# Kernel optimization log

Measured on AMD Instinct MI355X. Metric: run time of the kernel, lower is better.

The kernel has to match this reference:

```python
import jax, jax.numpy as jnp
import numpy as np

B = 64
IN_FEATURES = 20000
OUT_FEATURES = 2000  # out_features * K with K=1
N_EDGES = 2_000_000


def setup_inputs() -> dict:
    key = jax.random.key(0)
    k1, k2, k3 = jax.random.split(key, 3)
    input = jax.random.normal(k1, (B, IN_FEATURES), dtype=jnp.float32)
    # col 0: input neuron index, col 1: output neuron index (both < 2000, valid for both ranges)
    sparse_mask = jax.random.randint(k2, (N_EDGES, 2), 0, OUT_FEATURES, dtype=jnp.int64)
    weight = jax.random.normal(k3, (N_EDGES,), dtype=jnp.float32)
    bias = jnp.zeros((OUT_FEATURES,), dtype=jnp.float32)
    return {"input": input, "sparse_mask": sparse_mask, "weight": weight, "bias": bias}


def reference(input, sparse_mask, weight, bias):
    # gather: [B, E]
    src = input[:, sparse_mask[:, 0]] * weight[None, :]
    # scatter-add per-edge contributions into output neurons
    out = jnp.zeros((input.shape[0], OUT_FEATURES), dtype=input.dtype)
    out = out.at[:, sparse_mask[:, 1]].add(src)
    return out + bias
```

## Files before the change

### kernel.cpp

```cpp
#include <hip/hip_runtime.h>


#define ROWS8 8
#define NB 256
#define NSEGP 512
#define SCAP 32
#define OVB 32
#define E_PT 8
#define TPB_SC 512
#define SEGX (TPB_SC * E_PT)
#define PAD32 0xFFFFFFFFu

#define TILE_O 64
#define KS 64
#define SLICES 16
#define PSTRIDE 2048

__global__ __launch_bounds__(TPB_SC) void smw_scatter13(
    const int* __restrict__ mask, const float* __restrict__ wgt,
    unsigned* __restrict__ binned, int* __restrict__ counts,
    int2* __restrict__ ovfblk, int n_edges, int krows, int nbins, int nseg) {
    __shared__ int hist[NB];
    __shared__ int sflag;
    __shared__ int ovfc;
    extern __shared__ unsigned stage32[];
    const int tid = threadIdx.x;
    const int blk = blockIdx.x;
    const long long e0 = (long long)blk * SEGX;
    if (tid < NB) hist[tid] = 0;
    if (tid == 0) ovfc = 0;
    if (tid < 64) {
        unsigned v = (tid < n_edges) ? ((const unsigned*)mask)[2 * tid + 1] : 0u;
        unsigned long long bal = __ballot(v != 0u);
        if (tid == 0) sflag = (bal == 0ull) ? 1 : 0;
    }
    __syncthreads();
    const bool is64 = (sflag != 0);

    int ci[E_PT], co[E_PT]; float wv[E_PT];
    if (is64) {
        #pragma unroll
        for (int i = 0; i < E_PT; ++i) {
            long long e = e0 + (long long)i * TPB_SC + tid;
            ci[i] = -1; co[i] = 0;
            if (e < n_edges) { int4 mm = ((const int4*)mask)[e]; ci[i] = mm.x; co[i] = mm.z; }
        }
    } else {
        #pragma unroll
        for (int i = 0; i < E_PT; ++i) {
            long long e = e0 + (long long)i * TPB_SC + tid;
            ci[i] = -1; co[i] = 0;
            if (e < n_edges) { int2 mm = ((const int2*)mask)[e]; ci[i] = mm.x; co[i] = mm.y; }
        }
    }
    #pragma unroll
    for (int i = 0; i < E_PT; ++i) {
        long long e = e0 + (long long)i * TPB_SC + tid;
        wv[i] = (e < n_edges) ? wgt[e] : 0.0f;
    }

    #pragma unroll
    for (int i = 0; i < E_PT; ++i) {
        if ((unsigned)ci[i] < (unsigned)krows) {
            int b = ci[i] >> 3;
            int r = atomicAdd(&hist[b], 1);
            if (r < SCAP) {
                unsigned u  = __float_as_uint(wv[i]);
                unsigned bf = (u + 0x7FFFu + ((u >> 16) & 1u)) >> 16;
                unsigned key = (((unsigned)(ci[i] & 7)) << 11) | (unsigned)(co[i] & 0x7FF);
                stage32[b * SCAP + r] = (key << 16) | bf;
            } else {
                int j = atomicAdd(&ovfc, 1);
                if (j < OVB)
                    ovfblk[blk * OVB + j] =
                        make_int2((ci[i] << 16) | (co[i] & 0xFFFF),
                                  __float_as_int(wv[i]));
            }
        }
    }
    __syncthreads();
    const int grp = tid >> 4;
    const int ln  = tid & 15;
    for (int b = grp; b < nbins; b += (TPB_SC / 16)) {
        int c = hist[b]; if (c > SCAP) c = SCAP;
        int cp = (c + 7) & ~7;
        long long base = ((long long)b * nseg + blk) * SCAP;
        for (int k = ln; k < cp; k += 16)
            binned[base + k] = (k < c) ? stage32[b * SCAP + k] : PAD32;
        if (ln == 0) counts[b * NSEGP + blk] = cp;
    }
    if (tid == 0) {
        int oc = ovfc; if (oc > OVB) oc = OVB;
        counts[(NB - 1) * NSEGP + blk] = oc;
    }
}

__global__ __launch_bounds__(512) void smw_bin_build10(
    const unsigned* __restrict__ binned, const int* __restrict__ counts,
    const int2* __restrict__ ovfblk, float* __restrict__ W,
    int out_f, int krows, int nseg) {
    extern __shared__ float tile[];
    const int tid = threadIdx.x;
    const int bin = blockIdx.x;
    const int tile_elems = ROWS8 * out_f;
    {
        float4* t4 = (float4*)tile;
        int n4 = tile_elems >> 2;
        for (int t = tid; t < n4; t += 512) t4[t] = make_float4(0.f, 0.f, 0.f, 0.f);
    }
    __syncthreads();
    const int grp = tid >> 3;
    const int ln8 = tid & 7;
    for (int s = grp; s < nseg; s += 64) {
        int cp = counts[bin * NSEGP + s];
        const uint4* sp = (const uint4*)(binned + ((long long)bin * nseg + s) * SCAP);
        for (int j = ln8; j * 4 < cp; j += 8) {
            uint4 q = sp[j];
            #pragma unroll
            for (int t = 0; t < 4; ++t) {
                unsigned r = (t == 0) ? q.x : (t == 1) ? q.y : (t == 2) ? q.z : q.w;
                if ((int)r >= 0) {
                    unsigned key = r >> 16;
                    atomicAdd(&tile[(int)(key >> 11) * out_f + (int)(key & 0x7FFu)],
                              __uint_as_float((r & 0xFFFFu) << 16));
                }
            }
        }
    }
    for (int s = tid; s < nseg; s += 512) {
        int oc = counts[(NB - 1) * NSEGP + s];
        for (int j = 0; j < oc; ++j) {
            int2 r = ovfblk[s * OVB + j];
            int ci = ((unsigned)r.x) >> 16;
            if ((ci >> 3) == bin)
                atomicAdd(&tile[(ci & 7) * out_f + (r.x & 0xFFFF)],
                          __int_as_float(r.y));
        }
    }
    __syncthreads();
    #pragma unroll
    for (int r = 0; r < ROWS8; ++r) {
        int row = bin * ROWS8 + r;
        if (row >= krows) break;
        float* dst = W + (long long)row * out_f;
        const float* s = tile + r * out_f;
        for (int c = tid * 4; c < out_f; c += 2048)
            *(float4*)&dst[c] = *(const float4*)&s[c];
    }
}

__device__ __forceinline__ void smw_load_a(float4 (&r)[4], const float* __restrict__ A,
                                           int k0, int in_features, int krows,
                                           int Bsz, int tid) {
    #pragma unroll
    for (int t = 0; t < 4; ++t) {
        int idx = t * 256 + tid;
        int b = idx >> 4;
        int c4 = (idx & 15) * 4;
        int gi = k0 + c4;
        float4 v = make_float4(0.f, 0.f, 0.f, 0.f);
        if (b < Bsz) {
            const float* src = A + (long long)b * in_features + gi;
            if (gi + 3 < krows) v = *(const float4*)src;
            else {
                if (gi + 0 < krows) v.x = src[0];
                if (gi + 1 < krows) v.y = src[1];
                if (gi + 2 < krows) v.z = src[2];
                if (gi + 3 < krows) v.w = src[3];
            }
        }
        r[t] = v;
    }
}

__device__ __forceinline__ void smw_load_w(float4 (&r)[4], const float* __restrict__ W,
                                           int k0, int o_base, int out_f, int krows,
                                           int tid) {
    #pragma unroll
    for (int t = 0; t < 4; ++t) {
        int idx = t * 256 + tid;
        int rr = idx >> 4;
        int c4 = (idx & 15) * 4;
        int gi = k0 + rr;
        int go = o_base + c4;
        float4 v = make_float4(0.f, 0.f, 0.f, 0.f);
        if (gi < krows) {
            const float* src = W + (long long)gi * out_f + go;
            if (go + 3 < out_f) v = *(const float4*)src;
            else {
                if (go + 0 < out_f) v.x = src[0];
                if (go + 1 < out_f) v.y = src[1];
                if (go + 2 < out_f) v.z = src[2];
                if (go + 3 < out_f) v.w = src[3];
            }
        }
        r[t] = v;
    }
}

__global__ __launch_bounds__(256) void smw_gemm6(
    const float* __restrict__ A, const float* __restrict__ W,
    float* __restrict__ partial, int in_features, int out_f, int krows, int Bsz) {
    __shared__ float As[64][KS + 4];
    __shared__ float Ws[KS][TILE_O];
    const int tid = threadIdx.x;
    const int tx = tid & 15;
    const int ty = tid >> 4;
    const int o_base = blockIdx.x * TILE_O;
    const int k0a = blockIdx.y * 2 * KS;
    const int k0b = k0a + KS;

    float4 ra[4], rw[4];
    smw_load_a(ra, A, k0a, in_features, krows, Bsz, tid);
    smw_load_w(rw, W, k0a, o_base, out_f, krows, tid);
    #pragma unroll
    for (int t = 0; t < 4; ++t) {
        int idx = t * 256 + tid;
        *(float4*)&As[idx >> 4][(idx & 15) * 4] = ra[t];
        *(float4*)&Ws[idx >> 4][(idx & 15) * 4] = rw[t];
    }
    smw_load_a(ra, A, k0b, in_features, krows, Bsz, tid);
    smw_load_w(rw, W, k0b, o_base, out_f, krows, tid);
    __syncthreads();

    float acc[4][4] = {};
    #pragma unroll 8
    for (int i = 0; i < KS; ++i) {
        float4 w4 = *(const float4*)&Ws[i][tx * 4];
        float a[4];
        #pragma unroll
        for (int r = 0; r < 4; ++r) a[r] = As[ty * 4 + r][i];
        #pragma unroll
        for (int r = 0; r < 4; ++r) {
            acc[r][0] += a[r] * w4.x;
            acc[r][1] += a[r] * w4.y;
            acc[r][2] += a[r] * w4.z;
            acc[r][3] += a[r] * w4.w;
        }
    }
    __syncthreads();
    #pragma unroll
    for (int t = 0; t < 4; ++t) {
        int idx = t * 256 + tid;
        *(float4*)&As[idx >> 4][(idx & 15) * 4] = ra[t];
        *(float4*)&Ws[idx >> 4][(idx & 15) * 4] = rw[t];
    }
    __syncthreads();
    #pragma unroll 8
    for (int i = 0; i < KS; ++i) {
        float4 w4 = *(const float4*)&Ws[i][tx * 4];
        float a[4];
        #pragma unroll
        for (int r = 0; r < 4; ++r) a[r] = As[ty * 4 + r][i];
        #pragma unroll
        for (int r = 0; r < 4; ++r) {
            acc[r][0] += a[r] * w4.x;
            acc[r][1] += a[r] * w4.y;
            acc[r][2] += a[r] * w4.z;
            acc[r][3] += a[r] * w4.w;
        }
    }

    float* P = partial + (long long)blockIdx.y * 64 * PSTRIDE;
    #pragma unroll
    for (int r = 0; r < 4; ++r) {
        int b = ty * 4 + r;
        if (b < Bsz)
            *(float4*)&P[(long long)b * PSTRIDE + o_base + tx * 4] =
                make_float4(acc[r][0], acc[r][1], acc[r][2], acc[r][3]);
    }
}

__global__ void smw_reduce3(const float* __restrict__ partial,
                            const float* __restrict__ bias,
                            float* __restrict__ out, int out_f, int Bsz, int total4) {
    int idx = blockIdx.x * blockDim.x + threadIdx.x;
    if (idx >= total4) return;
    const int of4 = out_f >> 2;
    int b = idx / of4, o4 = idx - b * of4;
    const float4* B4 = (const float4*)bias;
    const float4* P4 = (const float4*)partial;
    float4 acc = B4[o4];
    #pragma unroll
    for (int s = 0; s < SLICES; ++s) {
        float4 v = P4[((long long)s * 64 + b) * (PSTRIDE >> 2) + o4];
        acc.x += v.x; acc.y += v.y; acc.z += v.z; acc.w += v.w;
    }
    ((float4*)out)[idx] = acc;
}

__global__ void smw_detect(const unsigned int* __restrict__ m, int* __restrict__ flag) {
    if (blockIdx.x == 0 && threadIdx.x == 0) {
        unsigned int orv = 0u;
        for (int k = 0; k < 64; ++k) orv |= m[2 * k + 1];
        *flag = (orv == 0u) ? 1 : 0;
    }
}

__global__ void smw_build_fb(const int* __restrict__ mask, const float* __restrict__ wgt,
                             float* __restrict__ W, const int* __restrict__ flag,
                             int n_edges, int out_f) {
    int e = blockIdx.x * blockDim.x + threadIdx.x;
    if (e >= n_edges) return;
    int ci, co;
    if (*flag) {
        const long long* m64 = (const long long*)mask;
        ci = (int)m64[2 * (long long)e];
        co = (int)m64[2 * (long long)e + 1];
    } else {
        ci = mask[2 * e]; co = mask[2 * e + 1];
    }
    atomicAdd(&W[(long long)ci * out_f + co], wgt[e]);
}

__global__ void smw_init_out_fb(float* __restrict__ out, const float* __restrict__ bias,
                                int total, int out_f) {
    int idx = blockIdx.x * blockDim.x + threadIdx.x;
    if (idx < total) out[idx] = bias[idx % out_f];
}

__global__ __launch_bounds__(256) void smw_gemm_fb(
    const float* __restrict__ A, const float* __restrict__ W,
    float* __restrict__ out, int in_features, int out_f, int krows,
    int n_chunks, int Bsz) {
    __shared__ float As[64][36];
    __shared__ float Ws[32][64];
    const int tid = threadIdx.x;
    const int tx = tid & 15;
    const int ty = tid >> 4;
    const int o_base = blockIdx.x * 64;
    float acc[4][4] = {};
    for (int c = blockIdx.y; c < n_chunks; c += 8) {
        const int i0 = c * 32;
        __syncthreads();
        #pragma unroll
        for (int k = 0; k < 8; ++k) {
            int idx = k * 256 + tid;
            int i = idx & 31;
            int b = idx >> 5;
            float v = 0.0f;
            int gi = i0 + i;
            if (b < Bsz && gi < in_features) v = A[(long long)b * in_features + gi];
            As[b][i] = v;
        }
        #pragma unroll
        for (int k = 0; k < 8; ++k) {
            int idx = k * 256 + tid;
            int o = idx & 63;
            int i = idx >> 6;
            int gi = i0 + i;
            int go = o_base + o;
            Ws[i][o] = (gi < krows && go < out_f) ? W[(long long)gi * out_f + go] : 0.0f;
        }
        __syncthreads();
        #pragma unroll
        for (int i = 0; i < 32; ++i) {
            float4 w4 = *(const float4*)(&Ws[i][tx * 4]);
            float a[4];
            #pragma unroll
            for (int r = 0; r < 4; ++r) a[r] = As[ty * 4 + r][i];
            #pragma unroll
            for (int r = 0; r < 4; ++r) {
                acc[r][0] += a[r] * w4.x;
                acc[r][1] += a[r] * w4.y;
                acc[r][2] += a[r] * w4.z;
                acc[r][3] += a[r] * w4.w;
            }
        }
    }
    #pragma unroll
    for (int r = 0; r < 4; ++r) {
        int b = ty * 4 + r;
        if (b >= Bsz) continue;
        #pragma unroll
        for (int cc = 0; cc < 4; ++cc) {
            int o = o_base + tx * 4 + cc;
            if (o < out_f) atomicAdd(&out[(long long)b * out_f + o], acc[r][cc]);
        }
    }
}

static inline size_t align_up(size_t x, size_t a) { return (x + a - 1) & ~(a - 1); }

extern "C" void kernel_launch(void* const* d_in, const int* in_sizes, int n_in,
                              void* d_out, int out_size, void* d_ws, size_t ws_size,
                              hipStream_t stream) {
    const float* input = (const float*)d_in[0];
    const int*   mask  = (const int*)d_in[1];
    const float* wgt   = (const float*)d_in[2];
    const float* bias  = (const float*)d_in[3];
    float* out = (float*)d_out;

    const int out_f   = in_sizes[3];
    const int n_edges = in_sizes[2];
    const int Bsz     = out_size / out_f;
    const int in_features = in_sizes[0] / Bsz;
    const int krows   = out_f;
    const int nbins   = (krows + ROWS8 - 1) / ROWS8;
    const int nseg    = (n_edges + SEGX - 1) / SEGX;
    const int n_ot    = (out_f + TILE_O - 1) / TILE_O;

    size_t W_bytes      = align_up((size_t)krows * out_f * 4, 1024);
    size_t binned_bytes = align_up((size_t)nbins * nseg * SCAP * 4, 1024);
    size_t part_bytes   = align_up((size_t)SLICES * 64 * PSTRIDE * 4, 1024);
    size_t union_bytes  = binned_bytes > part_bytes ? binned_bytes : part_bytes;
    size_t counts_bytes = align_up((size_t)NB * NSEGP * 4, 1024);
    size_t ovf_bytes    = align_up((size_t)nseg * OVB * 8, 1024);
    size_t need_fast = W_bytes + union_bytes + counts_bytes + ovf_bytes + 1024;

    char* p = (char*)d_ws;
    float*    W       = (float*)p;
    unsigned* binned  = (unsigned*)(p + W_bytes);
    float*    partial = (float*)(p + W_bytes);
    int*      counts  = (int*)(p + W_bytes + union_bytes);
    int2*     ovfblk  = (int2*)(p + W_bytes + union_bytes + counts_bytes);

    const size_t sc_lds = (size_t)nbins * SCAP * 4;
    const size_t bb_lds = (size_t)ROWS8 * out_f * 4;
    const bool fast = (ws_size >= need_fast) && out_f <= 2048 && (out_f & 3) == 0 &&
                      krows <= 2048 && nbins <= 250 && Bsz <= 64 && n_edges >= 1 &&
                      n_ot <= 32 && nseg <= NSEGP && sc_lds <= 64000 &&
                      bb_lds <= 65536 && (out_size & 3) == 0;

    if (fast) {
        smw_scatter13<<<nseg, TPB_SC, sc_lds, stream>>>(mask, wgt, binned, counts,
                                                        ovfblk, n_edges, krows,
                                                        nbins, nseg);
        smw_bin_build10<<<nbins, 512, bb_lds, stream>>>(binned, counts, ovfblk, W,
                                                        out_f, krows, nseg);
        dim3 grid(n_ot, SLICES);
        smw_gemm6<<<grid, 256, 0, stream>>>(input, W, partial, in_features, out_f,
                                            krows, Bsz);
        int total4 = out_size >> 2;
        smw_reduce3<<<(total4 + 255) / 256, 256, 0, stream>>>(partial, bias, out,
                                                              out_f, Bsz, total4);
    } else {
        int* flag_fb = (int*)(p + (size_t)krows * out_f * 4);
        hipMemsetAsync(d_ws, 0, (size_t)krows * out_f * 4, stream);
        smw_detect<<<1, 64, 0, stream>>>((const unsigned int*)mask, flag_fb);
        smw_build_fb<<<(n_edges + 255) / 256, 256, 0, stream>>>(mask, wgt, W, flag_fb,
                                                                n_edges, out_f);
        smw_init_out_fb<<<(out_size + 255) / 256, 256, 0, stream>>>(out, bias, out_size, out_f);
        const int n_chunks = (krows + 31) / 32;
        dim3 grid((out_f + 63) / 64, 8);
        smw_gemm_fb<<<grid, 256, 0, stream>>>(input, W, out, in_features, out_f,
                                              krows, n_chunks, Bsz);
    }
}
```

Baseline: 49.66 us.

## Halve bin rows to double build blocks and deepen GEMM K per block

Shrinks each bin from 8 to 4 input rows (512 bins, capacity 16 per segment), doubling the number of bin-build workgroups and halving their LDS tile so more blocks run per CU. The GEMM now processes 4 K-chunks per block with register prefetch and 8 slices instead of 16, which cuts partial-sum traffic and the work left for the reduce. The risks are more overflow entries from the smaller per-bin capacity, and fewer GEMM blocks, which lowers parallelism in that kernel.

```diff
diff --git a/kernel.cpp b/kernel.cpp
--- a/kernel.cpp
+++ b/kernel.cpp
@@ -1,10 +1,10 @@
 #include <hip/hip_runtime.h>
 
 
-#define ROWS8 8
-#define NB 256
+#define ROWSB 4
+#define NB 512
 #define NSEGP 512
-#define SCAP 32
+#define SCAP 16
 #define OVB 32
 #define E_PT 8
 #define TPB_SC 512
@@ -13,10 +13,11 @@
 
 #define TILE_O 64
 #define KS 64
-#define SLICES 16
+#define SLICES 8
+#define NCH 4
 #define PSTRIDE 2048
 
-__global__ __launch_bounds__(TPB_SC) void smw_scatter13(
+__global__ __launch_bounds__(TPB_SC) void smw_scatter14(
     const int* __restrict__ mask, const float* __restrict__ wgt,
     unsigned* __restrict__ binned, int* __restrict__ counts,
     int2* __restrict__ ovfblk, int n_edges, int krows, int nbins, int nseg) {
@@ -62,12 +63,12 @@
     #pragma unroll
     for (int i = 0; i < E_PT; ++i) {
         if ((unsigned)ci[i] < (unsigned)krows) {
-            int b = ci[i] >> 3;
+            int b = ci[i] >> 2;
             int r = atomicAdd(&hist[b], 1);
             if (r < SCAP) {
                 unsigned u  = __float_as_uint(wv[i]);
                 unsigned bf = (u + 0x7FFFu + ((u >> 16) & 1u)) >> 16;
-                unsigned key = (((unsigned)(ci[i] & 7)) << 11) | (unsigned)(co[i] & 0x7FF);
+                unsigned key = (((unsigned)(ci[i] & 3)) << 11) | (unsigned)(co[i] & 0x7FF);
                 stage32[b * SCAP + r] = (key << 16) | bf;
             } else {
                 int j = atomicAdd(&ovfc, 1);
@@ -85,8 +86,8 @@
         int c = hist[b]; if (c > SCAP) c = SCAP;
         int cp = (c + 7) & ~7;
         long long base = ((long long)b * nseg + blk) * SCAP;
-        for (int k = ln; k < cp; k += 16)
-            binned[base + k] = (k < c) ? stage32[b * SCAP + k] : PAD32;
+        if (ln < cp)
+            binned[base + ln] = (ln < c) ? stage32[b * SCAP + ln] : PAD32;
         if (ln == 0) counts[b * NSEGP + blk] = cp;
     }
     if (tid == 0) {
@@ -95,27 +96,26 @@
     }
 }
 
-__global__ __launch_bounds__(512) void smw_bin_build10(
+__global__ __launch_bounds__(512) void smw_bin_build11(
     const unsigned* __restrict__ binned, const int* __restrict__ counts,
     const int2* __restrict__ ovfblk, float* __restrict__ W,
     int out_f, int krows, int nseg) {
     extern __shared__ float tile[];
     const int tid = threadIdx.x;
     const int bin = blockIdx.x;
-    const int tile_elems = ROWS8 * out_f;
+    const int tile_elems = ROWSB * out_f;
     {
         float4* t4 = (float4*)tile;
         int n4 = tile_elems >> 2;
         for (int t = tid; t < n4; t += 512) t4[t] = make_float4(0.f, 0.f, 0.f, 0.f);
     }
     __syncthreads();
-    const int grp = tid >> 3;
-    const int ln8 = tid & 7;
-    for (int s = grp; s < nseg; s += 64) {
+    const int grp = tid >> 2;
+    const int ln4 = tid & 3;
+    for (int s = grp; s < nseg; s += 128) {
         int cp = counts[bin * NSEGP + s];
-        const uint4* sp = (const uint4*)(binned + ((long long)bin * nseg + s) * SCAP);
-        for (int j = ln8; j * 4 < cp; j += 8) {
-            uint4 q = sp[j];
+        if (ln4 * 4 < cp) {
+            uint4 q = ((const uint4*)(binned + ((long long)bin * nseg + s) * SCAP))[ln4];
             #pragma unroll
             for (int t = 0; t < 4; ++t) {
                 unsigned r = (t == 0) ? q.x : (t == 1) ? q.y : (t == 2) ? q.z : q.w;
@@ -132,15 +132,15 @@
         for (int j = 0; j < oc; ++j) {
             int2 r = ovfblk[s * OVB + j];
             int ci = ((unsigned)r.x) >> 16;
-            if ((ci >> 3) == bin)
-                atomicAdd(&tile[(ci & 7) * out_f + (r.x & 0xFFFF)],
+            if ((ci >> 2) == bin)
+                atomicAdd(&tile[(ci & 3) * out_f + (r.x & 0xFFFF)],
                           __int_as_float(r.y));
         }
     }
     __syncthreads();
     #pragma unroll
-    for (int r = 0; r < ROWS8; ++r) {
-        int row = bin * ROWS8 + r;
+    for (int r = 0; r < ROWSB; ++r) {
+        int row = bin * ROWSB + r;
         if (row >= krows) break;
         float* dst = W + (long long)row * out_f;
         const float* s = tile + r * out_f;
@@ -198,7 +198,7 @@
     }
 }
 
-__global__ __launch_bounds__(256) void smw_gemm6(
+__global__ __launch_bounds__(256) void smw_gemm7(
     const float* __restrict__ A, const float* __restrict__ W,
     float* __restrict__ partial, int in_features, int out_f, int krows, int Bsz) {
     __shared__ float As[64][KS + 4];
@@ -207,57 +207,51 @@
     const int tx = tid & 15;
     const int ty = tid >> 4;
     const int o_base = blockIdx.x * TILE_O;
-    const int k0a = blockIdx.y * 2 * KS;
-    const int k0b = k0a + KS;
+    const int k0 = blockIdx.y * (NCH * KS);
 
     float4 ra[4], rw[4];
-    smw_load_a(ra, A, k0a, in_features, krows, Bsz, tid);
-    smw_load_w(rw, W, k0a, o_base, out_f, krows, tid);
+    smw_load_a(ra, A, k0, in_features, krows, Bsz, tid);
+    smw_load_w(rw, W, k0, o_base, out_f, krows, tid);
     #pragma unroll
     for (int t = 0; t < 4; ++t) {
         int idx = t * 256 + tid;
         *(float4*)&As[idx >> 4][(idx & 15) * 4] = ra[t];
         *(float4*)&Ws[idx >> 4][(idx & 15) * 4] = rw[t];
     }
-    smw_load_a(ra, A, k0b, in_features, krows, Bsz, tid);
-    smw_load_w(rw, W, k0b, o_base, out_f, krows, tid);
+    smw_load_a(ra, A, k0 + KS, in_features, krows, Bsz, tid);
+    smw_load_w(rw, W, k0 + KS, o_base, out_f, krows, tid);
     __syncthreads();
 
     float acc[4][4] = {};
-    #pragma unroll 8
-    for (int i = 0; i < KS; ++i) {
-        float4 w4 = *(const float4*)&Ws[i][tx * 4];
-        float a[4];
-        #pragma unroll
-        for (int r = 0; r < 4; ++r) a[r] = As[ty * 4 + r][i];
-        #pragma unroll
-        for (int r = 0; r < 4; ++r) {
-            acc[r][0] += a[r] * w4.x;
-            acc[r][1] += a[r] * w4.y;
-            acc[r][2] += a[r] * w4.z;
-            acc[r][3] += a[r] * w4.w;
-        }
-    }
-    __syncthreads();
-    #pragma unroll
-    for (int t = 0; t < 4; ++t) {
-        int idx = t * 256 + tid;
-        *(float4*)&As[idx >> 4][(idx & 15) * 4] = ra[t];
-        *(float4*)&Ws[idx >> 4][(idx & 15) * 4] = rw[t];
-    }
-    __syncthreads();
-    #pragma unroll 8
-    for (int i = 0; i < KS; ++i) {
-        float4 w4 = *(const float4*)&Ws[i][tx * 4];
-        float a[4];
-        #pragma unroll
-        for (int r = 0; r < 4; ++r) a[r] = As[ty * 4 + r][i];
-        #pragma unroll
-        for (int r = 0; r < 4; ++r) {
-            acc[r][0] += a[r] * w4.x;
-            acc[r][1] += a[r] * w4.y;
-            acc[r][2] += a[r] * w4.z;
-            acc[r][3] += a[r] * w4.w;
+    #pragma unroll
+    for (int ch = 0; ch < NCH; ++ch) {
+        #pragma unroll 8
+        for (int i = 0; i < KS; ++i) {
+            float4 w4 = *(const float4*)&Ws[i][tx * 4];
+            float a[4];
+            #pragma unroll
+            for (int r = 0; r < 4; ++r) a[r] = As[ty * 4 + r][i];
+            #pragma unroll
+            for (int r = 0; r < 4; ++r) {
+                acc[r][0] += a[r] * w4.x;
+                acc[r][1] += a[r] * w4.y;
+                acc[r][2] += a[r] * w4.z;
+                acc[r][3] += a[r] * w4.w;
+            }
+        }
+        if (ch < NCH - 1) {
+            __syncthreads();
+            #pragma unroll
+            for (int t = 0; t < 4; ++t) {
+                int idx = t * 256 + tid;
+                *(float4*)&As[idx >> 4][(idx & 15) * 4] = ra[t];
+                *(float4*)&Ws[idx >> 4][(idx & 15) * 4] = rw[t];
+            }
+            if (ch < NCH - 2) {
+                smw_load_a(ra, A, k0 + (ch + 2) * KS, in_features, krows, Bsz, tid);
+                smw_load_w(rw, W, k0 + (ch + 2) * KS, o_base, out_f, krows, tid);
+            }
+            __syncthreads();
         }
     }
 
@@ -271,7 +265,7 @@
     }
 }
 
-__global__ void smw_reduce3(const float* __restrict__ partial,
+__global__ void smw_reduce4(const float* __restrict__ partial,
                             const float* __restrict__ bias,
                             float* __restrict__ out, int out_f, int Bsz, int total4) {
     int idx = blockIdx.x * blockDim.x + threadIdx.x;
@@ -396,7 +390,7 @@
     const int Bsz     = out_size / out_f;
     const int in_features = in_sizes[0] / Bsz;
     const int krows   = out_f;
-    const int nbins   = (krows + ROWS8 - 1) / ROWS8;
+    const int nbins   = (krows + ROWSB - 1) / ROWSB;
     const int nseg    = (n_edges + SEGX - 1) / SEGX;
     const int n_ot    = (out_f + TILE_O - 1) / TILE_O;
 
@@ -416,23 +410,23 @@
     int2*     ovfblk  = (int2*)(p + W_bytes + union_bytes + counts_bytes);
 
     const size_t sc_lds = (size_t)nbins * SCAP * 4;
-    const size_t bb_lds = (size_t)ROWS8 * out_f * 4;
+    const size_t bb_lds = (size_t)ROWSB * out_f * 4;
     const bool fast = (ws_size >= need_fast) && out_f <= 2048 && (out_f & 3) == 0 &&
-                      krows <= 2048 && nbins <= 250 && Bsz <= 64 && n_edges >= 1 &&
+                      krows <= 2048 && nbins <= NB - 1 && Bsz <= 64 && n_edges >= 1 &&
                       n_ot <= 32 && nseg <= NSEGP && sc_lds <= 64000 &&
-                      bb_lds <= 65536 && (out_size & 3) == 0;
+                      bb_lds <= 32768 && (out_size & 3) == 0;
 
     if (fast) {
-        smw_scatter13<<<nseg, TPB_SC, sc_lds, stream>>>(mask, wgt, binned, counts,
+        smw_scatter14<<<nseg, TPB_SC, sc_lds, stream>>>(mask, wgt, binned, counts,
                                                         ovfblk, n_edges, krows,
                                                         nbins, nseg);
-        smw_bin_build10<<<nbins, 512, bb_lds, stream>>>(binned, counts, ovfblk, W,
+        smw_bin_build11<<<nbins, 512, bb_lds, stream>>>(binned, counts, ovfblk, W,
                                                         out_f, krows, nseg);
         dim3 grid(n_ot, SLICES);
-        smw_gemm6<<<grid, 256, 0, stream>>>(input, W, partial, in_features, out_f,
+        smw_gemm7<<<grid, 256, 0, stream>>>(input, W, partial, in_features, out_f,
                                             krows, Bsz);
         int total4 = out_size >> 2;
-        smw_reduce3<<<(total4 + 255) / 256, 256, 0, stream>>>(partial, bias, out,
+        smw_reduce4<<<(total4 + 255) / 256, 256, 0, stream>>>(partial, bias, out,
                                                               out_f, Bsz, total4);
     } else {
         int* flag_fb = (int*)(p + (size_t)krows * out_f * 4);
```

New measurement: 54.54 us. 1.1x slower.
